# Performance work log

Hardware: AMD Instinct MI355X
Metric: run time of the kernel (lower is better)

Reference implementation:

```python
import jax, jax.numpy as jnp
import numpy as np
import math

B, S = 4, 1024
D_MODEL = 512
N_HEADS = 8
D_HEAD = D_MODEL // N_HEADS
D_FF = 2048
D_K_NEIGHBOR = 512.0
EPS_NORM = 1e-5
GN_EPS = 1e-5
LAMBDA_INIT = 0.8 - 0.6 * math.exp(-0.3 * 0.0)  # layer_idx = 0 -> 0.2


def _rmsnorm(x, w, eps=EPS_NORM):
    return x * jax.lax.rsqrt(jnp.mean(x * x, axis=-1, keepdims=True) + eps) * w


def _group_norm(x, gamma, beta):
    # x: [B, S, D]; torch GroupNorm(n_heads, d_model) applied on [B, D, S]:
    # normalize each (batch, group) over (d_head * S) elements, per-channel affine.
    b, s, d = x.shape
    xg = x.transpose(0, 2, 1).reshape(b, N_HEADS, D_HEAD, s)
    mean = xg.mean(axis=(2, 3), keepdims=True)
    var = ((xg - mean) ** 2).mean(axis=(2, 3), keepdims=True)
    xn = ((xg - mean) * jax.lax.rsqrt(var + GN_EPS)).reshape(b, d, s)
    xn = xn * gamma[None, :, None] + beta[None, :, None]
    return xn.transpose(0, 2, 1)


def setup_inputs() -> dict:
    key = jax.random.key(0)
    ks = jax.random.split(key, 20)
    sd = 1.0 / math.sqrt(D_MODEL)
    sdf = 1.0 / math.sqrt(D_FF)
    f32 = jnp.float32
    return {
        'x': jax.random.normal(ks[0], (B, S, D_MODEL), f32),
        'src_padding_mask': jax.random.randint(ks[1], (B, S), 0, 2).astype(jnp.int32),
        'learned_lambda': jnp.asarray(LAMBDA_INIT, f32),
        'wq_w': (jax.random.normal(ks[2], (D_MODEL, 2 * D_MODEL), f32) * sd),
        'wq_b': jnp.zeros((2 * D_MODEL,), f32),
        'wk_w': (jax.random.normal(ks[3], (D_MODEL, 2 * D_MODEL), f32) * sd),
        'wk_b': jnp.zeros((2 * D_MODEL,), f32),
        'wv_w': (jax.random.normal(ks[4], (D_MODEL, D_MODEL), f32) * sd),
        'wv_b': jnp.zeros((D_MODEL,), f32),
        'out_w': (jax.random.normal(ks[5], (D_MODEL, D_MODEL), f32) * sd),
        'out_b': jnp.zeros((D_MODEL,), f32),
        'gn_gamma': jnp.ones((D_MODEL,), f32),
        'gn_beta': jnp.zeros((D_MODEL,), f32),
        'aq_w': (jax.random.normal(ks[6], (D_MODEL, D_MODEL), f32) * sd),
        'aq_b': jnp.zeros((D_MODEL,), f32),
        'ak_w': (jax.random.normal(ks[7], (D_MODEL, D_MODEL), f32) * sd),
        'ak_b': jnp.zeros((D_MODEL,), f32),
        'wg_w': (jax.random.normal(ks[8], (D_MODEL, D_FF), f32) * sd),
        'w1_w': (jax.random.normal(ks[9], (D_MODEL, D_FF), f32) * sd),
        'w2_w': (jax.random.normal(ks[10], (D_FF, D_MODEL), f32) * sdf),
        'norm1_w': jnp.ones((D_MODEL,), f32),
        'norm2_w': jnp.ones((D_MODEL,), f32),
    }


def reference(x, src_padding_mask, learned_lambda,
              wq_w, wq_b, wk_w, wk_b, wv_w, wv_b, out_w, out_b,
              gn_gamma, gn_beta, aq_w, aq_b, ak_w, ak_b,
              wg_w, w1_w, w2_w, norm1_w, norm2_w):
    b, s, d = x.shape
    x_norm = _rmsnorm(x, norm1_w)

    # ---- neighbor affinity (layer_idx = 0 -> a = a_hat) ----
    Q = x_norm @ aq_w + aq_b
    K = x_norm @ ak_w + ak_b
    s_fwd = jnp.sum(Q[:, :-1] * K[:, 1:], axis=-1) / D_K_NEIGHBOR   # [B, S-1]
    s_bwd = jnp.sum(Q[:, 1:] * K[:, :-1], axis=-1) / D_K_NEIGHBOR
    a = 0.5 * (jax.nn.sigmoid(s_fwd) + jax.nn.sigmoid(s_bwd))        # [B, S-1]

    # ---- hierarchical mask: C[i,j] = prod(a[i:j]) = exp(L[j]-L[i]), symmetric ----
    # L is non-increasing (a in (0,1)), so prod(a[i:j]) = exp(-|L[i]-L[j]|); diag = 1.
    L = jnp.concatenate([jnp.zeros((b, 1), x.dtype), jnp.cumsum(jnp.log(a), axis=1)], axis=1)  # [B, S]
    C = jnp.exp(-jnp.abs(L[:, :, None] - L[:, None, :]))[:, None]   # [B,1,S,S]

    # ---- differential multi-head attention ----
    qp = x_norm @ wq_w + wq_b   # [B,S,2D]
    kp = x_norm @ wk_w + wk_b
    heads = lambda t: t.reshape(b, s, N_HEADS, D_HEAD).transpose(0, 2, 1, 3)
    q1, q2 = heads(qp[..., :D_MODEL]), heads(qp[..., D_MODEL:])
    k1, k2 = heads(kp[..., :D_MODEL]), heads(kp[..., D_MODEL:])
    v = heads(x_norm @ wv_w + wv_b)
    scale = 1.0 / math.sqrt(D_HEAD)
    sc1 = jnp.einsum('bhqd,bhkd->bhqk', q1, k1) * scale
    sc2 = jnp.einsum('bhqd,bhkd->bhqk', q2, k2) * scale
    pad = (src_padding_mask == 0)[:, None, None, :]
    sc1 = jnp.where(pad, -1e9, sc1)
    sc2 = jnp.where(pad, -1e9, sc2)
    aw1 = jax.nn.softmax(sc1, axis=-1)
    aw2 = jax.nn.softmax(sc2, axis=-1)
    comb = C * (aw1 - learned_lambda * aw2)
    ctx = jnp.einsum('bhqk,bhkd->bhqd', comb, v)
    ctx = ctx.transpose(0, 2, 1, 3).reshape(b, s, D_MODEL)
    ctx = _group_norm(ctx, gn_gamma, gn_beta) * (1.0 - LAMBDA_INIT)
    attn_out = ctx @ out_w + out_b

    # ---- residual + SwiGLU FFN (dropout = identity in eval) ----
    h = x + attn_out
    hn = _rmsnorm(h, norm2_w)
    ffn = (jax.nn.silu(hn @ wg_w) * (hn @ w1_w)) @ w2_w
    return h + ffn
```

## Files before the change

kernel.cpp:

```cpp
#include <hip/hip_runtime.h>
#include <math.h>

#define Bn 4
#define Sn 1024
#define DM 512
#define NH 8
#define DFF 2048
#define QKVN 2560

typedef __attribute__((ext_vector_type(8))) __bf16 bf16x8;
typedef __attribute__((ext_vector_type(2))) __bf16 bf16x2;
typedef __attribute__((ext_vector_type(4))) float f32x4;

#define MB (1u<<20)

__device__ __forceinline__ void gl_lds16(const void* g, void* l) {
    __builtin_amdgcn_global_load_lds(
        (const __attribute__((address_space(1))) void*)g,
        (__attribute__((address_space(3))) void*)l, 16, 0, 0);
}

struct TransBatch { const float* src[4]; __bf16* dst[4]; };

__global__ __launch_bounds__(256)
void transpose_kernel(TransBatch tb, int K, int N) {
    const float* w = tb.src[blockIdx.z];
    __bf16* wT = tb.dst[blockIdx.z];
    __shared__ float tile[32][33];
    int n0 = blockIdx.x * 32, k0 = blockIdx.y * 32;
    int tx = threadIdx.x, ty = threadIdx.y;
#pragma unroll
    for (int i = 0; i < 4; ++i)
        tile[ty + 8 * i][tx] = w[(size_t)(k0 + ty + 8 * i) * N + n0 + tx];
    __syncthreads();
#pragma unroll
    for (int i = 0; i < 4; ++i)
        wT[(size_t)(n0 + ty + 8 * i) * K + k0 + tx] = (__bf16)tile[tx][ty + 8 * i];
}

__global__ __launch_bounds__(256)
void pack_biases(const float* aq_b, const float* ak_b, const float* wq_b,
                 const float* wk_b, const float* wv_b,
                 float* aqk_b, float* qkv_b) {
    int t = blockIdx.x * 256 + threadIdx.x;
    if (t < 512) aqk_b[t] = aq_b[t];
    else if (t < 1024) aqk_b[t] = ak_b[t - 512];
    else if (t < 2048) qkv_b[t - 1024] = wq_b[t - 1024];
    else if (t < 3072) qkv_b[1024 + t - 2048] = wk_b[t - 2048];
    else if (t < 3584) qkv_b[2048 + t - 3072] = wv_b[t - 3072];
}

__global__ __launch_bounds__(256)
void rmsnorm_kernel(const float* __restrict__ x, const float* __restrict__ w,
                    __bf16* __restrict__ out) {
    int row = blockIdx.x;
    const float* xr = x + (size_t)row * DM;
    int t = threadIdx.x;
    float2 v = *(const float2*)&xr[2 * t];
    float ss = v.x * v.x + v.y * v.y;
#pragma unroll
    for (int off = 32; off; off >>= 1) ss += __shfl_xor(ss, off);
    __shared__ float red[4];
    int wid = t >> 6;
    if ((t & 63) == 0) red[wid] = ss;
    __syncthreads();
    float tot = red[0] + red[1] + red[2] + red[3];
    float rinv = rsqrtf(tot / (float)DM + 1e-5f);
    bf16x2 o;
    o[0] = (__bf16)(v.x * rinv * w[2 * t]);
    o[1] = (__bf16)(v.y * rinv * w[2 * t + 1]);
    *(bf16x2*)&out[(size_t)row * DM + 2 * t] = o;
}

template<int BM, int BN, int EPI>
__global__ __launch_bounds__(256)
void gemm_bf16(const __bf16* __restrict__ A, const __bf16* __restrict__ BT,
               const float* __restrict__ bias, const float* __restrict__ res,
               void* __restrict__ out, int M, int N, int K) {
    __shared__ __align__(16) char AsB[BM * 64];
    __shared__ __align__(16) char BsB[BN * 64];
    const int t = threadIdx.x;
    const int w = t >> 6, l = t & 63, c = l & 15, g = l >> 4;
    const int wr = w >> 1, wc = w & 1;
    const int bm = blockIdx.y * BM, bn = blockIdx.x * BN;
    constexpr int HM = BM / 2, WM = BM / 32, HN = BN / 2, WN = BN / 32;
    f32x4 acc[WM][WN];
#pragma unroll
    for (int m = 0; m < WM; ++m)
#pragma unroll
        for (int n = 0; n < WN; ++n) acc[m][n] = (f32x4){0.f, 0.f, 0.f, 0.f};
    const int srow = t >> 2;
    const int kcol = ((t & 3) ^ ((t >> 3) & 3)) << 3;
    const __bf16* Ap = A + (size_t)(bm + srow) * K + kcol;
    const __bf16* Bp = BT + (size_t)(bn + srow) * K + kcol;
    const int sw = (g ^ ((c >> 1) & 3)) << 4;
    for (int k0 = 0; k0 < K; k0 += 32) {
        gl_lds16(Ap + k0, AsB + t * 16);
        if constexpr (BM == 128) gl_lds16(Ap + (size_t)64 * K + k0, AsB + 4096 + t * 16);
        gl_lds16(Bp + k0, BsB + t * 16);
        if constexpr (BN == 128) gl_lds16(Bp + (size_t)64 * K + k0, BsB + 4096 + t * 16);
        __syncthreads();
        bf16x8 af[WM], bf_[WN];
#pragma unroll
        for (int m = 0; m < WM; ++m)
            af[m] = *(const bf16x8*)(AsB + (wr * HM + m * 16 + c) * 64 + sw);
#pragma unroll
        for (int n = 0; n < WN; ++n)
            bf_[n] = *(const bf16x8*)(BsB + (wc * HN + n * 16 + c) * 64 + sw);
#pragma unroll
        for (int m = 0; m < WM; ++m)
#pragma unroll
            for (int n = 0; n < WN; ++n)
                acc[m][n] = __builtin_amdgcn_mfma_f32_16x16x32_bf16(af[m], bf_[n], acc[m][n], 0, 0, 0);
        __syncthreads();
    }
#pragma unroll
    for (int m = 0; m < WM; ++m)
#pragma unroll
        for (int n = 0; n < WN; ++n) {
            int rowb = bm + wr * HM + m * 16 + 4 * g;
            int col = bn + wc * HN + n * 16 + c;
            float bv = bias ? bias[col] : 0.f;
#pragma unroll
            for (int r = 0; r < 4; ++r) {
                size_t idx = (size_t)(rowb + r) * N + col;
                float val = acc[m][n][r] + bv;
                if constexpr (EPI == 0) {
                    ((__bf16*)out)[idx] = (__bf16)val;
                } else {
                    if (res) val += res[idx];
                    ((float*)out)[idx] = val;
                }
            }
        }
}

__global__ __launch_bounds__(256)
void gemm_swiglu(const __bf16* __restrict__ A, const __bf16* __restrict__ GT,
                 const __bf16* __restrict__ UT, __bf16* __restrict__ out,
                 int M, int N, int K) {
    __shared__ __align__(16) char AsB[128 * 64];
    __shared__ __align__(16) char GsB[128 * 64];
    __shared__ __align__(16) char UsB[128 * 64];
    const int t = threadIdx.x;
    const int w = t >> 6, l = t & 63, c = l & 15, g = l >> 4;
    const int wr = w >> 1, wc = w & 1;
    const int bm = blockIdx.y * 128, bn = blockIdx.x * 128;
    f32x4 accg[4][4], accu[4][4];
#pragma unroll
    for (int m = 0; m < 4; ++m)
#pragma unroll
        for (int n = 0; n < 4; ++n) {
            accg[m][n] = (f32x4){0.f, 0.f, 0.f, 0.f};
            accu[m][n] = (f32x4){0.f, 0.f, 0.f, 0.f};
        }
    const int srow = t >> 2;
    const int kcol = ((t & 3) ^ ((t >> 3) & 3)) << 3;
    const __bf16* Ap = A + (size_t)(bm + srow) * K + kcol;
    const __bf16* Gp = GT + (size_t)(bn + srow) * K + kcol;
    const __bf16* Up = UT + (size_t)(bn + srow) * K + kcol;
    const int sw = (g ^ ((c >> 1) & 3)) << 4;
    for (int k0 = 0; k0 < K; k0 += 32) {
        gl_lds16(Ap + k0, AsB + t * 16);
        gl_lds16(Ap + (size_t)64 * K + k0, AsB + 4096 + t * 16);
        gl_lds16(Gp + k0, GsB + t * 16);
        gl_lds16(Gp + (size_t)64 * K + k0, GsB + 4096 + t * 16);
        gl_lds16(Up + k0, UsB + t * 16);
        gl_lds16(Up + (size_t)64 * K + k0, UsB + 4096 + t * 16);
        __syncthreads();
        bf16x8 af[4], gf[4], uf[4];
#pragma unroll
        for (int m = 0; m < 4; ++m)
            af[m] = *(const bf16x8*)(AsB + (wr * 64 + m * 16 + c) * 64 + sw);
#pragma unroll
        for (int n = 0; n < 4; ++n) {
            gf[n] = *(const bf16x8*)(GsB + (wc * 64 + n * 16 + c) * 64 + sw);
            uf[n] = *(const bf16x8*)(UsB + (wc * 64 + n * 16 + c) * 64 + sw);
        }
#pragma unroll
        for (int m = 0; m < 4; ++m)
#pragma unroll
            for (int n = 0; n < 4; ++n) {
                accg[m][n] = __builtin_amdgcn_mfma_f32_16x16x32_bf16(af[m], gf[n], accg[m][n], 0, 0, 0);
                accu[m][n] = __builtin_amdgcn_mfma_f32_16x16x32_bf16(af[m], uf[n], accu[m][n], 0, 0, 0);
            }
        __syncthreads();
    }
#pragma unroll
    for (int m = 0; m < 4; ++m)
#pragma unroll
        for (int n = 0; n < 4; ++n) {
            int rowb = bm + wr * 64 + m * 16 + 4 * g;
            int col = bn + wc * 64 + n * 16 + c;
#pragma unroll
            for (int r = 0; r < 4; ++r) {
                float gv = accg[m][n][r];
                float uv = accu[m][n][r];
                float sg = gv / (1.f + __expf(-gv));
                out[(size_t)(rowb + r) * N + col] = (__bf16)(sg * uv);
            }
        }
}

__global__ __launch_bounds__(256)
void affinity_dots(const __bf16* __restrict__ aqk, float* __restrict__ la) {
    int i = blockIdx.x * 256 + threadIdx.x;
    int b = blockIdx.y;
    if (i >= Sn - 1) { la[b * Sn + i] = 0.f; return; }
    const __bf16* Qi = aqk + (size_t)(b * Sn + i) * 1024;
    const __bf16* Ki = Qi + 512;
    float sf = 0.f, sb = 0.f;
#pragma unroll 4
    for (int d = 0; d < DM / 8; ++d) {
        bf16x8 q0 = *(const bf16x8*)(Qi + d * 8);
        bf16x8 q1 = *(const bf16x8*)(Qi + 1024 + d * 8);
        bf16x8 k0 = *(const bf16x8*)(Ki + d * 8);
        bf16x8 k1 = *(const bf16x8*)(Ki + 1024 + d * 8);
#pragma unroll
        for (int j = 0; j < 8; ++j) {
            sf += (float)q0[j] * (float)k1[j];
            sb += (float)q1[j] * (float)k0[j];
        }
    }
    sf *= (1.f / 512.f);
    sb *= (1.f / 512.f);
    float a = 0.5f * (1.f / (1.f + __expf(-sf)) + 1.f / (1.f + __expf(-sb)));
    la[b * Sn + i] = __logf(a);
}

__global__ __launch_bounds__(256)
void scan_kernel(const float* __restrict__ la, float* __restrict__ L) {
    int b = blockIdx.x, j = threadIdx.x;
    __shared__ float sc[256];
    float4 v = *(const float4*)&la[b * Sn + 4 * j];
    float s0 = v.x, s1 = s0 + v.y, s2 = s1 + v.z, s3 = s2 + v.w;
    sc[j] = s3;
    __syncthreads();
    for (int off = 1; off < 256; off <<= 1) {
        float add = (j >= off) ? sc[j - off] : 0.f;
        __syncthreads();
        sc[j] += add;
        __syncthreads();
    }
    float base = sc[j] - s3;
    if (j == 0) L[b * Sn] = 0.f;
    L[b * Sn + 4 * j + 1] = base + s0;
    L[b * Sn + 4 * j + 2] = base + s1;
    L[b * Sn + 4 * j + 3] = base + s2;
    if (4 * j + 4 < Sn) L[b * Sn + 4 * j + 4] = base + s3;
}

__global__ __launch_bounds__(512)
void attn_mfma(const __bf16* __restrict__ qkv, const float* __restrict__ L,
               const int* __restrict__ mask, const float* __restrict__ lam_p,
               float* __restrict__ ctx) {
    int x = blockIdx.x;
    int xcd = x & 7, idx = x >> 3;
    int bh = xcd * 4 + (idx >> 4);
    int qb = idx & 15;
    int b = bh >> 3, h = bh & 7;
    const int t = threadIdx.x;
    const int w = t >> 6, l = t & 63, c = l & 15, g = l >> 4;
    const int mat = w >> 2, ws = w & 3;

    __shared__ __align__(16) char KldsB[64 * 256];
    __shared__ __align__(16) char VtB[64 * 128];
    __shared__ __align__(16) char PldsB[2][64 * 128];
    __shared__ float Lk_s[64];
    __shared__ float msk_s[64];
    __shared__ float fs_s[2][64];
    __shared__ float ls_s[2][64];

    const int q0 = qb * 64;
    const int qg = q0 + 16 * ws + c;
    float Lq = L[b * Sn + qg];
    float lam = lam_p[0];
    bf16x8 qf[2];
#pragma unroll
    for (int dh = 0; dh < 2; ++dh)
        qf[dh] = *(const bf16x8*)(qkv + (size_t)(b * Sn + qg) * QKVN + mat * 512 + h * 64 + dh * 32 + g * 8);
    f32x4 O[4];
#pragma unroll
    for (int nd = 0; nd < 4; ++nd) O[nd] = (f32x4){0.f, 0.f, 0.f, 0.f};
    float m_run = -INFINITY;
    float l_run = 0.f;
    const int cs = c & 7;

    for (int kt = 0; kt < 16; ++kt) {
        const size_t kbase = (size_t)(b * Sn + kt * 64);
#pragma unroll
        for (int rep = 0; rep < 2; ++rep) {
            int u = t & 255;
            int rr = (t >> 8) + 2 * rep;
            int krow = rr * 16 + (u >> 4);
            int km = (u >> 3) & 1;
            int lg = (u & 7) ^ (krow & 7);
            gl_lds16(qkv + (kbase + krow) * QKVN + 1024 + km * 512 + h * 64 + lg * 8,
                     KldsB + rr * 4096 + u * 16);
        }
        {
            int k = t & 63, dg = t >> 6;
            bf16x8 val = *(const bf16x8*)(qkv + (kbase + k) * QKVN + 2048 + h * 64 + dg * 8);
#pragma unroll
            for (int j = 0; j < 8; ++j)
                *(__bf16*)(VtB + (dg * 8 + j) * 128 + ((((k >> 3) ^ j) << 4) | ((k & 7) << 1))) = val[j];
        }
        if (t < 64) {
            Lk_s[t] = L[b * Sn + kt * 64 + t];
            msk_s[t] = (float)mask[b * Sn + kt * 64 + t];
        }
        __syncthreads();
        float Cv[16];
        unsigned mbits = 0;
#pragma unroll
        for (int kf = 0; kf < 4; ++kf)
#pragma unroll
            for (int r = 0; r < 4; ++r) {
                int kk = kf * 16 + 4 * g + r;
                Cv[kf * 4 + r] = __expf(-fabsf(Lq - Lk_s[kk]));
                mbits |= (msk_s[kk] != 0.f ? 1u : 0u) << (kf * 4 + r);
            }
        f32x4 s[4];
        __builtin_amdgcn_s_setprio(1);
#pragma unroll
        for (int kf = 0; kf < 4; ++kf) {
            f32x4 a = (f32x4){0.f, 0.f, 0.f, 0.f};
#pragma unroll
            for (int dh = 0; dh < 2; ++dh) {
                bf16x8 kfr = *(const bf16x8*)(KldsB + (kf * 16 + c) * 256 + (mat * 8 + ((dh * 4 + g) ^ cs)) * 16);
                a = __builtin_amdgcn_mfma_f32_16x16x32_bf16(kfr, qf[dh], a, 0, 0, 0);
            }
            s[kf] = a;
        }
        __builtin_amdgcn_s_setprio(0);
        float tm = -INFINITY;
#pragma unroll
        for (int kf = 0; kf < 4; ++kf)
#pragma unroll
            for (int r = 0; r < 4; ++r) {
                float sv = ((mbits >> (kf * 4 + r)) & 1u) ? s[kf][r] * 0.125f : -1e9f;
                s[kf][r] = sv;
                tm = fmaxf(tm, sv);
            }
        tm = fmaxf(tm, __shfl_xor(tm, 16));
        tm = fmaxf(tm, __shfl_xor(tm, 32));
        float mn = fmaxf(m_run, tm);
        float f = __expf(m_run - mn);
        m_run = mn;
        if (g == 0) fs_s[mat][16 * ws + c] = f;
        float es = 0.f;
#pragma unroll
        for (int kf = 0; kf < 4; ++kf) {
            bf16x2 p01, p23;
            float e0 = __expf(s[kf][0] - mn);
            float e1 = __expf(s[kf][1] - mn);
            float e2 = __expf(s[kf][2] - mn);
            float e3 = __expf(s[kf][3] - mn);
            es += (e0 + e1) + (e2 + e3);
            p01[0] = (__bf16)(e0 * Cv[kf * 4 + 0]);
            p01[1] = (__bf16)(e1 * Cv[kf * 4 + 1]);
            p23[0] = (__bf16)(e2 * Cv[kf * 4 + 2]);
            p23[1] = (__bf16)(e3 * Cv[kf * 4 + 3]);
            char* pb = PldsB[mat] + (16 * ws + c) * 128 + (((kf * 2 + (g >> 1)) ^ cs) << 4) + ((g & 1) << 3);
            *(bf16x2*)pb = p01;
            *(bf16x2*)(pb + 4) = p23;
        }
        es += __shfl_xor(es, 16);
        es += __shfl_xor(es, 32);
        l_run = l_run * f + es;
        __syncthreads();
        f32x4 fv = *(const f32x4*)&fs_s[mat][16 * ws + 4 * g];
#pragma unroll
        for (int nd = 0; nd < 4; ++nd) O[nd] *= fv;
        __builtin_amdgcn_s_setprio(1);
#pragma unroll
        for (int kh = 0; kh < 2; ++kh) {
            bf16x8 pa = *(const bf16x8*)(PldsB[mat] + (16 * ws + c) * 128 + (((kh * 4 + g) ^ cs) << 4));
#pragma unroll
            for (int nd = 0; nd < 4; ++nd) {
                bf16x8 vb = *(const bf16x8*)(VtB + (nd * 16 + c) * 128 + (((kh * 4 + g) ^ cs) << 4));
                O[nd] = __builtin_amdgcn_mfma_f32_16x16x32_bf16(pa, vb, O[nd], 0, 0, 0);
            }
        }
        __builtin_amdgcn_s_setprio(0);
        __syncthreads();
    }
    if (g == 0) ls_s[mat][16 * ws + c] = l_run;
    __syncthreads();
    f32x4 lv = *(const f32x4*)&ls_s[mat][16 * ws + 4 * g];
#pragma unroll
    for (int nd = 0; nd < 4; ++nd)
#pragma unroll
        for (int r = 0; r < 4; ++r) O[nd][r] /= lv[r];
    float* Pf = (float*)PldsB;
    if (mat == 1) {
#pragma unroll
        for (int nd = 0; nd < 4; ++nd)
#pragma unroll
            for (int r = 0; r < 4; ++r)
                Pf[(16 * ws + 4 * g + r) * 64 + nd * 16 + c] = O[nd][r];
    }
    __syncthreads();
    if (mat == 0) {
#pragma unroll
        for (int nd = 0; nd < 4; ++nd)
#pragma unroll
            for (int r = 0; r < 4; ++r) {
                float val = O[nd][r] - lam * Pf[(16 * ws + 4 * g + r) * 64 + nd * 16 + c];
                int q = q0 + 16 * ws + 4 * g + r;
                ctx[(size_t)(b * Sn + q) * DM + h * 64 + nd * 16 + c] = val;
            }
    }
}

__global__ __launch_bounds__(256)
void gn_stats(const float* __restrict__ ctx, float* __restrict__ stats) {
    int b = blockIdx.x >> 3, h = blockIdx.x & 7;
    int s0 = blockIdx.y * 128;
    int t = threadIdx.x;
    float sum = 0.f, sq = 0.f;
    for (int i = t; i < 128 * 32; i += 256) {
        int s = s0 + (i >> 5), dp = (i & 31) * 2;
        float2 vv = *(const float2*)&ctx[(size_t)(b * Sn + s) * DM + h * 64 + dp];
        sum += vv.x + vv.y;
        sq += vv.x * vv.x + vv.y * vv.y;
    }
#pragma unroll
    for (int off = 32; off; off >>= 1) {
        sum += __shfl_xor(sum, off);
        sq += __shfl_xor(sq, off);
    }
    __shared__ float rs[4], rq[4];
    int wid = t >> 6;
    if ((t & 63) == 0) { rs[wid] = sum; rq[wid] = sq; }
    __syncthreads();
    if (t == 0) {
        atomicAdd(&stats[blockIdx.x * 2], rs[0] + rs[1] + rs[2] + rs[3]);
        atomicAdd(&stats[blockIdx.x * 2 + 1], rq[0] + rq[1] + rq[2] + rq[3]);
    }
}

__global__ __launch_bounds__(256)
void gn_apply(const float* __restrict__ ctx, const float* __restrict__ stats,
              const float* __restrict__ gamma, const float* __restrict__ beta,
              __bf16* __restrict__ out) {
    int row = blockIdx.x;
    int b = row >> 10;
    int t = threadIdx.x;
    int dpair = t * 2;
    int h = dpair >> 6;
    float mean = stats[(b * 8 + h) * 2] * (1.f / 65536.f);
    float msq = stats[(b * 8 + h) * 2 + 1] * (1.f / 65536.f);
    float rinv = rsqrtf(msq - mean * mean + 1e-5f);
    size_t off_ = (size_t)row * DM + dpair;
    float2 vv = *(const float2*)&ctx[off_];
    bf16x2 o;
    o[0] = (__bf16)(((vv.x - mean) * rinv * gamma[dpair] + beta[dpair]) * 0.8f);
    o[1] = (__bf16)(((vv.y - mean) * rinv * gamma[dpair + 1] + beta[dpair + 1]) * 0.8f);
    *(bf16x2*)&out[off_] = o;
}

extern "C" void kernel_launch(void* const* d_in, const int* in_sizes, int n_in,
                              void* d_out, int out_size, void* d_ws, size_t ws_size,
                              hipStream_t stream) {
    const float* x        = (const float*)d_in[0];
    const int*   mask     = (const int*)d_in[1];
    const float* lam      = (const float*)d_in[2];
    const float* wq_w     = (const float*)d_in[3];
    const float* wq_b     = (const float*)d_in[4];
    const float* wk_w     = (const float*)d_in[5];
    const float* wk_b     = (const float*)d_in[6];
    const float* wv_w     = (const float*)d_in[7];
    const float* wv_b     = (const float*)d_in[8];
    const float* out_w    = (const float*)d_in[9];
    const float* out_b    = (const float*)d_in[10];
    const float* gn_gamma = (const float*)d_in[11];
    const float* gn_beta  = (const float*)d_in[12];
    const float* aq_w     = (const float*)d_in[13];
    const float* aq_b     = (const float*)d_in[14];
    const float* ak_w     = (const float*)d_in[15];
    const float* ak_b     = (const float*)d_in[16];
    const float* wg_w     = (const float*)d_in[17];
    const float* w1_w     = (const float*)d_in[18];
    const float* w2_w     = (const float*)d_in[19];
    const float* norm1_w  = (const float*)d_in[20];
    const float* norm2_w  = (const float*)d_in[21];

    char* ws = (char*)d_ws;
    __bf16* aqkT = (__bf16*)(ws + 0);
    __bf16* qkvT = (__bf16*)(ws + 1 * MB);
    __bf16* outT = (__bf16*)(ws + 7 * MB / 2);
    __bf16* wgT  = (__bf16*)(ws + 4 * MB);
    __bf16* w1T  = (__bf16*)(ws + 6 * MB);
    __bf16* w2T  = (__bf16*)(ws + 8 * MB);
    __bf16* xn   = (__bf16*)(ws + 10 * MB);
    __bf16* aqk  = (__bf16*)(ws + 14 * MB);
    __bf16* qkv  = (__bf16*)(ws + 22 * MB);
    float*  la   = (float*)(ws + 42 * MB);
    float*  Lb   = (float*)(ws + 42 * MB + 64 * 1024);
    float*  stats= (float*)(ws + 42 * MB + 128 * 1024);
    float*  aqk_b= (float*)(ws + 42 * MB + 192 * 1024);
    float*  qkv_b= (float*)(ws + 42 * MB + 256 * 1024);
    float*  ctx  = (float*)(ws + 43 * MB);
    __bf16* ctxb = (__bf16*)(ws + 51 * MB);
    float*  h    = (float*)(ws + 55 * MB);
    __bf16* hn   = (__bf16*)(ws + 14 * MB);
    __bf16* mid  = (__bf16*)(ws + 22 * MB);
    float*  outp = (float*)d_out;

    const int M = Bn * Sn;
    dim3 thr(32, 8);

    hipMemsetAsync(stats, 0, 64 * sizeof(float), stream);

    TransBatch ta = {{aq_w, ak_w, wv_w, out_w},
                     {aqkT, aqkT + 512 * 512, qkvT + (size_t)2048 * 512, outT}};
    transpose_kernel<<<dim3(16, 16, 4), thr, 0, stream>>>(ta, 512, 512);
    TransBatch tbq = {{wq_w, wk_w, nullptr, nullptr},
                      {qkvT, qkvT + (size_t)1024 * 512, nullptr, nullptr}};
    transpose_kernel<<<dim3(32, 16, 2), thr, 0, stream>>>(tbq, 512, 1024);
    TransBatch tc = {{wg_w, w1_w, nullptr, nullptr}, {wgT, w1T, nullptr, nullptr}};
    transpose_kernel<<<dim3(64, 16, 2), thr, 0, stream>>>(tc, 512, 2048);
    TransBatch td = {{w2_w, nullptr, nullptr, nullptr}, {w2T, nullptr, nullptr, nullptr}};
    transpose_kernel<<<dim3(16, 64, 1), thr, 0, stream>>>(td, 2048, 512);

    pack_biases<<<14, 256, 0, stream>>>(aq_b, ak_b, wq_b, wk_b, wv_b, aqk_b, qkv_b);

    rmsnorm_kernel<<<M, 256, 0, stream>>>(x, norm1_w, xn);

    gemm_bf16<64, 128, 0><<<dim3(8, 64), 256, 0, stream>>>(xn, aqkT, aqk_b, nullptr, aqk, M, 1024, 512);
    affinity_dots<<<dim3(4, 4), 256, 0, stream>>>(aqk, la);
    scan_kernel<<<Bn, 256, 0, stream>>>(la, Lb);

    gemm_bf16<128, 128, 0><<<dim3(20, 32), 256, 0, stream>>>(xn, qkvT, qkv_b, nullptr, qkv, M, QKVN, 512);

    attn_mfma<<<512, 512, 0, stream>>>(qkv, Lb, mask, lam, ctx);

    gn_stats<<<dim3(32, 8), 256, 0, stream>>>(ctx, stats);
    gn_apply<<<M, 256, 0, stream>>>(ctx, stats, gn_gamma, gn_beta, ctxb);

    gemm_bf16<64, 64, 1><<<dim3(8, 64), 256, 0, stream>>>(ctxb, outT, out_b, x, h, M, 512, 512);

    rmsnorm_kernel<<<M, 256, 0, stream>>>(h, norm2_w, hn);

    gemm_swiglu<<<dim3(16, 32), 256, 0, stream>>>(hn, wgT, w1T, mid, M, DFF, 512);

    gemm_bf16<64, 64, 1><<<dim3(8, 64), 256, 0, stream>>>(mid, w2T, nullptr, h, outp, M, 512, DFF);
}
```

Measured before the change: 352.1 us.

## Fuse affinity and QKV projections into one GEMM with transposed V output

Merges the affinity (aq/ak) and attention (q/k/v) projection GEMMs into a single GEMM over a concatenated weight matrix. The V columns are written transposed so the attention kernel can load them straight into LDS with async loads instead of scattering scalar stores. The affinity dot kernel is rewritten to use one wavefront per token with a shuffle reduction, raising its parallelism from 16 blocks. One __syncthreads is removed from the attention loop, which risks a race on fs_s if it was needed.

```diff
diff --git a/kernel.cpp b/kernel.cpp
--- a/kernel.cpp
+++ b/kernel.cpp
@@ -6,9 +6,10 @@
 #define DM 512
 #define NH 8
 #define DFF 2048
-#define QKVN 2560
+#define PROJN 3584
 
 typedef __attribute__((ext_vector_type(8))) __bf16 bf16x8;
+typedef __attribute__((ext_vector_type(4))) __bf16 bf16x4;
 typedef __attribute__((ext_vector_type(2))) __bf16 bf16x2;
 typedef __attribute__((ext_vector_type(4))) float f32x4;
 
@@ -40,14 +41,13 @@
 
 __global__ __launch_bounds__(256)
 void pack_biases(const float* aq_b, const float* ak_b, const float* wq_b,
-                 const float* wk_b, const float* wv_b,
-                 float* aqk_b, float* qkv_b) {
+                 const float* wk_b, const float* wv_b, float* proj_b) {
     int t = blockIdx.x * 256 + threadIdx.x;
-    if (t < 512) aqk_b[t] = aq_b[t];
-    else if (t < 1024) aqk_b[t] = ak_b[t - 512];
-    else if (t < 2048) qkv_b[t - 1024] = wq_b[t - 1024];
-    else if (t < 3072) qkv_b[1024 + t - 2048] = wk_b[t - 2048];
-    else if (t < 3584) qkv_b[2048 + t - 3072] = wv_b[t - 3072];
+    if (t < 512) proj_b[t] = aq_b[t];
+    else if (t < 1024) proj_b[t] = ak_b[t - 512];
+    else if (t < 2048) proj_b[t] = wq_b[t - 1024];
+    else if (t < 3072) proj_b[t] = wk_b[t - 2048];
+    else if (t < 3584) proj_b[t] = wv_b[t - 3072];
 }
 
 __global__ __launch_bounds__(256)
@@ -133,6 +133,75 @@
                 }
             }
         }
+}
+
+__global__ __launch_bounds__(256)
+void gemm_proj(const __bf16* __restrict__ A, const __bf16* __restrict__ BT,
+               const float* __restrict__ bias, __bf16* __restrict__ out,
+               __bf16* __restrict__ vT, int M, int N, int K) {
+    __shared__ __align__(16) char AsB[128 * 64];
+    __shared__ __align__(16) char BsB[128 * 64];
+    const int t = threadIdx.x;
+    const int w = t >> 6, l = t & 63, c = l & 15, g = l >> 4;
+    const int wr = w >> 1, wc = w & 1;
+    const int bm = blockIdx.y * 128, bn = blockIdx.x * 128;
+    f32x4 acc[4][4];
+#pragma unroll
+    for (int m = 0; m < 4; ++m)
+#pragma unroll
+        for (int n = 0; n < 4; ++n) acc[m][n] = (f32x4){0.f, 0.f, 0.f, 0.f};
+    const int srow = t >> 2;
+    const int kcol = ((t & 3) ^ ((t >> 3) & 3)) << 3;
+    const __bf16* Ap = A + (size_t)(bm + srow) * K + kcol;
+    const __bf16* Bp = BT + (size_t)(bn + srow) * K + kcol;
+    const int sw = (g ^ ((c >> 1) & 3)) << 4;
+    for (int k0 = 0; k0 < K; k0 += 32) {
+        gl_lds16(Ap + k0, AsB + t * 16);
+        gl_lds16(Ap + (size_t)64 * K + k0, AsB + 4096 + t * 16);
+        gl_lds16(Bp + k0, BsB + t * 16);
+        gl_lds16(Bp + (size_t)64 * K + k0, BsB + 4096 + t * 16);
+        __syncthreads();
+        bf16x8 af[4], bf_[4];
+#pragma unroll
+        for (int m = 0; m < 4; ++m)
+            af[m] = *(const bf16x8*)(AsB + (wr * 64 + m * 16 + c) * 64 + sw);
+#pragma unroll
+        for (int n = 0; n < 4; ++n)
+            bf_[n] = *(const bf16x8*)(BsB + (wc * 64 + n * 16 + c) * 64 + sw);
+#pragma unroll
+        for (int m = 0; m < 4; ++m)
+#pragma unroll
+            for (int n = 0; n < 4; ++n)
+                acc[m][n] = __builtin_amdgcn_mfma_f32_16x16x32_bf16(af[m], bf_[n], acc[m][n], 0, 0, 0);
+        __syncthreads();
+    }
+    if (bn < 3072) {
+#pragma unroll
+        for (int m = 0; m < 4; ++m)
+#pragma unroll
+            for (int n = 0; n < 4; ++n) {
+                int rowb = bm + wr * 64 + m * 16 + 4 * g;
+                int col = bn + wc * 64 + n * 16 + c;
+                float bv = bias[col];
+#pragma unroll
+                for (int r = 0; r < 4; ++r)
+                    out[(size_t)(rowb + r) * N + col] = (__bf16)(acc[m][n][r] + bv);
+            }
+    } else {
+#pragma unroll
+        for (int m = 0; m < 4; ++m)
+#pragma unroll
+            for (int n = 0; n < 4; ++n) {
+                int rowb = bm + wr * 64 + m * 16 + 4 * g;
+                int col = bn + wc * 64 + n * 16 + c;
+                float bv = bias[col];
+                int d = col - 3072;
+                bf16x4 pk;
+#pragma unroll
+                for (int r = 0; r < 4; ++r) pk[r] = (__bf16)(acc[m][n][r] + bv);
+                *(bf16x4*)(vT + (size_t)d * 4096 + rowb) = pk;
+            }
+    }
 }
 
 __global__ __launch_bounds__(256)
@@ -203,29 +272,36 @@
 }
 
 __global__ __launch_bounds__(256)
-void affinity_dots(const __bf16* __restrict__ aqk, float* __restrict__ la) {
-    int i = blockIdx.x * 256 + threadIdx.x;
+void affinity_dots(const __bf16* __restrict__ proj, float* __restrict__ la) {
     int b = blockIdx.y;
-    if (i >= Sn - 1) { la[b * Sn + i] = 0.f; return; }
-    const __bf16* Qi = aqk + (size_t)(b * Sn + i) * 1024;
-    const __bf16* Ki = Qi + 512;
+    int i = blockIdx.x * 4 + (threadIdx.x >> 6);
+    int l = threadIdx.x & 63;
+    if (i >= Sn - 1) { if (l == 0 && i < Sn) la[b * Sn + i] = 0.f; return; }
+    const __bf16* Qi  = proj + (size_t)(b * Sn + i) * PROJN;
+    const __bf16* Ki  = Qi + 512;
+    const __bf16* Qi1 = Qi + PROJN;
+    const __bf16* Ki1 = Ki + PROJN;
+    bf16x8 q0 = *(const bf16x8*)(Qi + l * 8);
+    bf16x8 k1 = *(const bf16x8*)(Ki1 + l * 8);
+    bf16x8 q1 = *(const bf16x8*)(Qi1 + l * 8);
+    bf16x8 k0 = *(const bf16x8*)(Ki + l * 8);
     float sf = 0.f, sb = 0.f;
-#pragma unroll 4
-    for (int d = 0; d < DM / 8; ++d) {
-        bf16x8 q0 = *(const bf16x8*)(Qi + d * 8);
-        bf16x8 q1 = *(const bf16x8*)(Qi + 1024 + d * 8);
-        bf16x8 k0 = *(const bf16x8*)(Ki + d * 8);
-        bf16x8 k1 = *(const bf16x8*)(Ki + 1024 + d * 8);
-#pragma unroll
-        for (int j = 0; j < 8; ++j) {
-            sf += (float)q0[j] * (float)k1[j];
-            sb += (float)q1[j] * (float)k0[j];
-        }
-    }
-    sf *= (1.f / 512.f);
-    sb *= (1.f / 512.f);
-    float a = 0.5f * (1.f / (1.f + __expf(-sf)) + 1.f / (1.f + __expf(-sb)));
-    la[b * Sn + i] = __logf(a);
+#pragma unroll
+    for (int j = 0; j < 8; ++j) {
+        sf += (float)q0[j] * (float)k1[j];
+        sb += (float)q1[j] * (float)k0[j];
+    }
+#pragma unroll
+    for (int off = 32; off; off >>= 1) {
+        sf += __shfl_xor(sf, off);
+        sb += __shfl_xor(sb, off);
+    }
+    if (l == 0) {
+        sf *= (1.f / 512.f);
+        sb *= (1.f / 512.f);
+        float a = 0.5f * (1.f / (1.f + __expf(-sf)) + 1.f / (1.f + __expf(-sb)));
+        la[b * Sn + i] = __logf(a);
+    }
 }
 
 __global__ __launch_bounds__(256)
@@ -251,9 +327,9 @@
 }
 
 __global__ __launch_bounds__(512)
-void attn_mfma(const __bf16* __restrict__ qkv, const float* __restrict__ L,
-               const int* __restrict__ mask, const float* __restrict__ lam_p,
-               float* __restrict__ ctx) {
+void attn_mfma(const __bf16* __restrict__ proj, const __bf16* __restrict__ vT,
+               const float* __restrict__ L, const int* __restrict__ mask,
+               const float* __restrict__ lam_p, float* __restrict__ ctx) {
     int x = blockIdx.x;
     int xcd = x & 7, idx = x >> 3;
     int bh = xcd * 4 + (idx >> 4);
@@ -278,7 +354,7 @@
     bf16x8 qf[2];
 #pragma unroll
     for (int dh = 0; dh < 2; ++dh)
-        qf[dh] = *(const bf16x8*)(qkv + (size_t)(b * Sn + qg) * QKVN + mat * 512 + h * 64 + dh * 32 + g * 8);
+        qf[dh] = *(const bf16x8*)(proj + (size_t)(b * Sn + qg) * PROJN + 1024 + mat * 512 + h * 64 + dh * 32 + g * 8);
     f32x4 O[4];
 #pragma unroll
     for (int nd = 0; nd < 4; ++nd) O[nd] = (f32x4){0.f, 0.f, 0.f, 0.f};
@@ -287,7 +363,7 @@
     const int cs = c & 7;
 
     for (int kt = 0; kt < 16; ++kt) {
-        const size_t kbase = (size_t)(b * Sn + kt * 64);
+        const int ktok = b * Sn + kt * 64;
 #pragma unroll
         for (int rep = 0; rep < 2; ++rep) {
             int u = t & 255;
@@ -295,19 +371,17 @@
             int krow = rr * 16 + (u >> 4);
             int km = (u >> 3) & 1;
             int lg = (u & 7) ^ (krow & 7);
-            gl_lds16(qkv + (kbase + krow) * QKVN + 1024 + km * 512 + h * 64 + lg * 8,
+            gl_lds16(proj + (size_t)(ktok + krow) * PROJN + 2048 + km * 512 + h * 64 + lg * 8,
                      KldsB + rr * 4096 + u * 16);
         }
         {
-            int k = t & 63, dg = t >> 6;
-            bf16x8 val = *(const bf16x8*)(qkv + (kbase + k) * QKVN + 2048 + h * 64 + dg * 8);
-#pragma unroll
-            for (int j = 0; j < 8; ++j)
-                *(__bf16*)(VtB + (dg * 8 + j) * 128 + ((((k >> 3) ^ j) << 4) | ((k & 7) << 1))) = val[j];
+            int row = t >> 3;
+            int lg = (t & 7) ^ (row & 7);
+            gl_lds16(vT + (size_t)(h * 64 + row) * 4096 + ktok + lg * 8, VtB + t * 16);
         }
         if (t < 64) {
-            Lk_s[t] = L[b * Sn + kt * 64 + t];
-            msk_s[t] = (float)mask[b * Sn + kt * 64 + t];
+            Lk_s[t] = L[ktok + t];
+            msk_s[t] = (float)mask[ktok + t];
         }
         __syncthreads();
         float Cv[16];
@@ -368,7 +442,6 @@
         es += __shfl_xor(es, 16);
         es += __shfl_xor(es, 32);
         l_run = l_run * f + es;
-        __syncthreads();
         f32x4 fv = *(const f32x4*)&fs_s[mat][16 * ws + 4 * g];
 #pragma unroll
         for (int nd = 0; nd < 4; ++nd) O[nd] *= fv;
@@ -487,26 +560,24 @@
     const float* norm2_w  = (const float*)d_in[21];
 
     char* ws = (char*)d_ws;
-    __bf16* aqkT = (__bf16*)(ws + 0);
-    __bf16* qkvT = (__bf16*)(ws + 1 * MB);
-    __bf16* outT = (__bf16*)(ws + 7 * MB / 2);
-    __bf16* wgT  = (__bf16*)(ws + 4 * MB);
-    __bf16* w1T  = (__bf16*)(ws + 6 * MB);
-    __bf16* w2T  = (__bf16*)(ws + 8 * MB);
-    __bf16* xn   = (__bf16*)(ws + 10 * MB);
-    __bf16* aqk  = (__bf16*)(ws + 14 * MB);
-    __bf16* qkv  = (__bf16*)(ws + 22 * MB);
-    float*  la   = (float*)(ws + 42 * MB);
-    float*  Lb   = (float*)(ws + 42 * MB + 64 * 1024);
-    float*  stats= (float*)(ws + 42 * MB + 128 * 1024);
-    float*  aqk_b= (float*)(ws + 42 * MB + 192 * 1024);
-    float*  qkv_b= (float*)(ws + 42 * MB + 256 * 1024);
-    float*  ctx  = (float*)(ws + 43 * MB);
-    __bf16* ctxb = (__bf16*)(ws + 51 * MB);
-    float*  h    = (float*)(ws + 55 * MB);
-    __bf16* hn   = (__bf16*)(ws + 14 * MB);
-    __bf16* mid  = (__bf16*)(ws + 22 * MB);
-    float*  outp = (float*)d_out;
+    __bf16* projT = (__bf16*)(ws + 0);
+    __bf16* outT  = (__bf16*)(ws + 7 * MB / 2);
+    __bf16* wgT   = (__bf16*)(ws + 4 * MB);
+    __bf16* w1T   = (__bf16*)(ws + 6 * MB);
+    __bf16* w2T   = (__bf16*)(ws + 8 * MB);
+    __bf16* xn    = (__bf16*)(ws + 10 * MB);
+    __bf16* proj  = (__bf16*)(ws + 14 * MB);
+    __bf16* vT    = (__bf16*)(ws + 42 * MB);
+    float*  la    = (float*)(ws + 46 * MB);
+    float*  Lb    = (float*)(ws + 46 * MB + 64 * 1024);
+    float*  stats = (float*)(ws + 46 * MB + 128 * 1024);
+    float*  proj_b= (float*)(ws + 46 * MB + 192 * 1024);
+    float*  ctx   = (float*)(ws + 47 * MB);
+    float*  h     = (float*)(ws + 55 * MB);
+    __bf16* ctxb  = (__bf16*)(ws + 10 * MB);
+    __bf16* mid   = (__bf16*)(ws + 14 * MB);
+    __bf16* hn    = (__bf16*)(ws + 42 * MB);
+    float*  outp  = (float*)d_out;
 
     const int M = Bn * Sn;
     dim3 thr(32, 8);
@@ -514,27 +585,26 @@
     hipMemsetAsync(stats, 0, 64 * sizeof(float), stream);
 
     TransBatch ta = {{aq_w, ak_w, wv_w, out_w},
-                     {aqkT, aqkT + 512 * 512, qkvT + (size_t)2048 * 512, outT}};
+                     {projT, projT + 512 * 512, projT + (size_t)3072 * 512, outT}};
     transpose_kernel<<<dim3(16, 16, 4), thr, 0, stream>>>(ta, 512, 512);
     TransBatch tbq = {{wq_w, wk_w, nullptr, nullptr},
-                      {qkvT, qkvT + (size_t)1024 * 512, nullptr, nullptr}};
+                      {projT + (size_t)1024 * 512, projT + (size_t)2048 * 512, nullptr, nullptr}};
     transpose_kernel<<<dim3(32, 16, 2), thr, 0, stream>>>(tbq, 512, 1024);
     TransBatch tc = {{wg_w, w1_w, nullptr, nullptr}, {wgT, w1T, nullptr, nullptr}};
     transpose_kernel<<<dim3(64, 16, 2), thr, 0, stream>>>(tc, 512, 2048);
     TransBatch td = {{w2_w, nullptr, nullptr, nullptr}, {w2T, nullptr, nullptr, nullptr}};
     transpose_kernel<<<dim3(16, 64, 1), thr, 0, stream>>>(td, 2048, 512);
 
-    pack_biases<<<14, 256, 0, stream>>>(aq_b, ak_b, wq_b, wk_b, wv_b, aqk_b, qkv_b);
+    pack_biases<<<14, 256, 0, stream>>>(aq_b, ak_b, wq_b, wk_b, wv_b, proj_b);
 
     rmsnorm_kernel<<<M, 256, 0, stream>>>(x, norm1_w, xn);
 
-    gemm_bf16<64, 128, 0><<<dim3(8, 64), 256, 0, stream>>>(xn, aqkT, aqk_b, nullptr, aqk, M, 1024, 512);
-    affinity_dots<<<dim3(4, 4), 256, 0, stream>>>(aqk, la);
+    gemm_proj<<<dim3(28, 32), 256, 0, stream>>>(xn, projT, proj_b, proj, vT, M, PROJN, 512);
+
+    affinity_dots<<<dim3(256, 4), 256, 0, stream>>>(proj, la);
     scan_kernel<<<Bn, 256, 0, stream>>>(la, Lb);
 
-    gemm_bf16<128, 128, 0><<<dim3(20, 32), 256, 0, stream>>>(xn, qkvT, qkv_b, nullptr, qkv, M, QKVN, 512);
-
-    attn_mfma<<<512, 512, 0, stream>>>(qkv, Lb, mask, lam, ctx);
+    attn_mfma<<<512, 512, 0, stream>>>(proj, vT, Lb, mask, lam, ctx);
 
     gn_stats<<<dim3(32, 8), 256, 0, stream>>>(ctx, stats);
     gn_apply<<<M, 256, 0, stream>>>(ctx, stats, gn_gamma, gn_beta, ctxb);
```

New measurement: 315.5 us. 1.12x faster.
